# Performance work log

Measured on AMD Instinct MI355X. Metric: run time of the kernel, lower is better.

The kernel has to match this reference:

```python
import jax, jax.numpy as jnp
import numpy as np

N_POINTS = 2_000_000
GRID = (128, 128, 128)
N_COMP = 3


def _bspline_weights(u):
    # cubic B-spline basis, returns tuple of 4 arrays shaped like u
    u2 = u * u
    u3 = u2 * u
    w0 = (1.0 - u) ** 3 / 6.0
    w1 = (3.0 * u3 - 6.0 * u2 + 4.0) / 6.0
    w2 = (-3.0 * u3 + 3.0 * u2 + 3.0 * u + 1.0) / 6.0
    w3 = u3 / 6.0
    return (w0, w1, w2, w3)


def setup_inputs() -> dict:
    key = jax.random.key(0)
    kx, ky, kz, kp = jax.random.split(key, 4)
    # query points uniform in the supported domain [-1, 1]
    x = jax.random.uniform(kx, (N_POINTS,), jnp.float32, -1.0, 1.0)
    y = jax.random.uniform(ky, (N_POINTS,), jnp.float32, -1.0, 1.0)
    z = jax.random.uniform(kz, (N_POINTS,), jnp.float32, -1.0, 1.0)
    phi_x = jax.random.normal(kp, (*GRID, N_COMP), jnp.float32)
    return {"x": x, "y": y, "z": z, "phi_x": phi_x}


def reference(x, y, z, phi_x):
    # BSplineField3d.vectorized_displacement with support_outside=True,
    # default support_range=None -> spacing = 2/(n-3), origin = -1 - spacing.
    nx, ny, nz, _ = phi_x.shape
    dx = 2.0 / (nx - 3)
    dy = 2.0 / (ny - 3)
    dz = 2.0 / (nz - 3)
    ox, oy, oz = -1.0 - dx, -1.0 - dy, -1.0 - dz

    u = (x - ox - dx) / dx
    v = (y - oy - dy) / dy
    w = (z - oz - dz) / dz
    ix = jnp.floor(u).astype(jnp.int32)
    iy = jnp.floor(v).astype(jnp.int32)
    iz = jnp.floor(w).astype(jnp.int32)
    u = u - ix
    v = v - iy
    w = w - iz

    wu = _bspline_weights(u)
    wv = _bspline_weights(v)
    ww = _bspline_weights(w)

    T = jnp.zeros((x.shape[0], phi_x.shape[-1]), dtype=x.dtype)
    # 64 fixed taps: gather from control grid at clamped indices, MAC.
    for l in range(4):
        ixl = jnp.clip(ix + l, 0, nx - 1)
        for m in range(4):
            iym = jnp.clip(iy + m, 0, ny - 1)
            wum = wu[l] * wv[m]
            for n in range(4):
                izn = jnp.clip(iz + n, 0, nz - 1)
                coef = wum * ww[n]  # [N]
                T = T + coef[:, None] * phi_x[ixl, iym, izn]  # gather [N, C]
    return T
```

## Files before the change

kernel.cpp:

```cpp
#include <hip/hip_runtime.h>


#define NBINS 4096
#define NBLK  256

__device__ __forceinline__ void bspline_w(float u, float& w0, float& w1,
                                          float& w2, float& w3) {
    const float u2 = u * u;
    const float u3 = u2 * u;
    const float t  = 1.0f - u;
    w0 = t * t * t * (1.0f / 6.0f);
    w1 = (3.0f * u3 - 6.0f * u2 + 4.0f) * (1.0f / 6.0f);
    w2 = (-3.0f * u3 + 3.0f * u2 + 3.0f * u + 1.0f) * (1.0f / 6.0f);
    w3 = u3 * (1.0f / 6.0f);
}

__device__ __forceinline__ int point_bin(float x, float y, float z) {
    const float dx = 2.0f / 125.0f;
    const float ox = -1.0f - dx;
    const int ix = (int)floorf((x - ox - dx) / dx);
    const int iy = (int)floorf((y - ox - dx) / dx);
    const int iz = (int)floorf((z - ox - dx) / dx);
    const int bx = min(max(ix, 0), 127) >> 3;
    const int by = min(max(iy, 0), 127) >> 3;
    const int bz = min(max(iz, 0), 127) >> 3;
    return (bx << 8) | (by << 4) | bz;
}

__global__ __launch_bounds__(256) void hist_kernel(
    const float* __restrict__ xs, const float* __restrict__ ys,
    const float* __restrict__ zs, unsigned* __restrict__ hist,
    int n, int chunk) {
    __shared__ unsigned h[NBINS];
    for (int j = threadIdx.x; j < NBINS; j += 256) h[j] = 0;
    __syncthreads();
    const int b = blockIdx.x;
    const int lo = b * chunk;
    const int hi = min(n, lo + chunk);
    for (int i = lo + threadIdx.x; i < hi; i += 256)
        atomicAdd(&h[point_bin(xs[i], ys[i], zs[i])], 1u);
    __syncthreads();
    for (int j = threadIdx.x; j < NBINS; j += 256) hist[b * NBINS + j] = h[j];
}

__global__ __launch_bounds__(256) void colscan_kernel(
    unsigned* __restrict__ hist, unsigned* __restrict__ total) {
    const int j = blockIdx.x * 256 + threadIdx.x;
    unsigned run = 0;
#pragma unroll 8
    for (int b = 0; b < NBLK; ++b) {
        const unsigned c = hist[b * NBINS + j];
        hist[b * NBINS + j] = run;
        run += c;
    }
    total[j] = run;
}

__global__ __launch_bounds__(1024) void scan_kernel(
    const unsigned* __restrict__ total, unsigned* __restrict__ binbase) {
    __shared__ unsigned sdata[1024];
    const int t = threadIdx.x;
    const unsigned v0 = total[4 * t + 0];
    const unsigned v1 = total[4 * t + 1];
    const unsigned v2 = total[4 * t + 2];
    const unsigned v3 = total[4 * t + 3];
    sdata[t] = v0 + v1 + v2 + v3;
    __syncthreads();
    for (int off = 1; off < 1024; off <<= 1) {
        unsigned x = (t >= off) ? sdata[t - off] : 0u;
        __syncthreads();
        sdata[t] += x;
        __syncthreads();
    }
    const unsigned ex = (t > 0) ? sdata[t - 1] : 0u;
    binbase[4 * t + 0] = ex;
    binbase[4 * t + 1] = ex + v0;
    binbase[4 * t + 2] = ex + v0 + v1;
    binbase[4 * t + 3] = ex + v0 + v1 + v2;
}

__global__ __launch_bounds__(256) void scatter_kernel(
    const float* __restrict__ xs, const float* __restrict__ ys,
    const float* __restrict__ zs, const unsigned* __restrict__ hist,
    const unsigned* __restrict__ binbase, float4* __restrict__ rec,
    int n, int chunk) {
    __shared__ unsigned off[NBINS];
    const int b = blockIdx.x;
    for (int j = threadIdx.x; j < NBINS; j += 256)
        off[j] = hist[b * NBINS + j] + binbase[j];
    __syncthreads();
    const int lo = b * chunk;
    const int hi = min(n, lo + chunk);
    for (int i = lo + threadIdx.x; i < hi; i += 256) {
        const float x = xs[i], y = ys[i], z = zs[i];
        const unsigned p = atomicAdd(&off[point_bin(x, y, z)], 1u);
        rec[p] = make_float4(x, y, z, __int_as_float(i));
    }
}

__global__ __launch_bounds__(512) void eval_kernel(
    const float4* __restrict__ rec, const unsigned* __restrict__ binbase,
    const unsigned* __restrict__ total, const float* __restrict__ phi,
    float* __restrict__ out) {
    const int bin = blockIdx.x;
    const unsigned cnt = total[bin];
    if (cnt == 0) return;
    const unsigned start = binbase[bin];

    const int gx0 = ((bin >> 8) & 15) << 3;
    const int gy0 = ((bin >> 4) & 15) << 3;
    const int gz0 = (bin & 15) << 3;

    __shared__ float raw[121 * 36];
    __shared__ float4 W4[121 * 24];

    if (gz0 <= 112) {
        for (int p = threadIdx.x; p < 121 * 9; p += 512) {
            const int row = p / 9;
            const int q   = p - row * 9;
            const int lx = row / 11, ly = row - (row / 11) * 11;
            const int gx = min(gx0 + lx, 127);
            const int gy = min(gy0 + ly, 127);
            const float* src =
                phi + (size_t)((gx * 128 + gy) * 128 + gz0) * 3 + q * 4;
            *reinterpret_cast<float4*>(&raw[row * 36 + q * 4]) =
                *reinterpret_cast<const float4*>(src);
        }
    } else {
        for (int p = threadIdx.x; p < 121 * 11; p += 512) {
            const int row = p / 11;
            const int zz  = p - row * 11;
            const int lx = row / 11, ly = row - (row / 11) * 11;
            const int gx = min(gx0 + lx, 127);
            const int gy = min(gy0 + ly, 127);
            const int z  = min(gz0 + zz, 127);
            const float* s = phi + (size_t)((gx * 128 + gy) * 128 + z) * 3;
            raw[row * 36 + zz * 3 + 0] = s[0];
            raw[row * 36 + zz * 3 + 1] = s[1];
            raw[row * 36 + zz * 3 + 2] = s[2];
        }
    }
    __syncthreads();

    for (int p = threadIdx.x; p < 121 * 24; p += 512) {
        const int row = p / 24;
        const int t   = p - row * 24;
        const int s   = t / 3;
        const int c   = t - 3 * s;
        const float* r = &raw[row * 36 + s * 3 + c];
        W4[p] = make_float4(r[0], r[3], r[6], r[9]);
    }
    __syncthreads();

    const float dx = 2.0f / 125.0f;
    const float ox = -1.0f - dx;

    for (unsigned k = start + threadIdx.x; k < start + cnt; k += 512) {
        const float4 r4 = rec[k];
        const int idx = __float_as_int(r4.w);

        const float U = (r4.x - ox - dx) / dx;
        const float V = (r4.y - ox - dx) / dx;
        const float Z = (r4.z - ox - dx) / dx;
        const float fu = floorf(U), fv = floorf(V), fw = floorf(Z);
        const int ix = (int)fu, iy = (int)fv, iz = (int)fw;
        const float u = U - fu, v = V - fv, w = Z - fw;

        float wu[4], wv[4], wz[4];
        bspline_w(u, wu[0], wu[1], wu[2], wu[3]);
        bspline_w(v, wv[0], wv[1], wv[2], wv[3]);
        bspline_w(w, wz[0], wz[1], wz[2], wz[3]);

        int izb = iz < 0 ? 0 : iz;
        const bool sh = izb > 124;
        if (sh) izb = 124;
        const float zw0 = sh ? 0.0f : wz[0];
        const float zw1 = sh ? wz[0] : wz[1];
        const float zw2 = sh ? wz[1] : wz[2];
        const float zw3 = sh ? (wz[2] + wz[3]) : wz[3];
        const int lzb3 = (izb - gz0) * 3;

        int lxi[4], lyi[4];
#pragma unroll
        for (int l = 0; l < 4; ++l) {
            lxi[l] = min(max(ix + l, 0), 127) - gx0;
            lyi[l] = min(max(iy + l, 0), 127) - gy0;
        }

        float acc0 = 0.0f, acc1 = 0.0f, acc2 = 0.0f;
#pragma unroll
        for (int l = 0; l < 4; ++l) {
            const int rowx = lxi[l] * 11;
#pragma unroll
            for (int m = 0; m < 4; ++m) {
                const int base = (rowx + lyi[m]) * 24 + lzb3;
                const float4 a  = W4[base + 0];
                const float4 bb = W4[base + 1];
                const float4 cc = W4[base + 2];
                const float wm = wu[l] * wv[m];
                const float c0 = wm * zw0;
                const float c1 = wm * zw1;
                const float c2 = wm * zw2;
                const float c3 = wm * zw3;
                acc0 = fmaf(c0, a.x, acc0);
                acc0 = fmaf(c1, a.y, acc0);
                acc0 = fmaf(c2, a.z, acc0);
                acc0 = fmaf(c3, a.w, acc0);
                acc1 = fmaf(c0, bb.x, acc1);
                acc1 = fmaf(c1, bb.y, acc1);
                acc1 = fmaf(c2, bb.z, acc1);
                acc1 = fmaf(c3, bb.w, acc1);
                acc2 = fmaf(c0, cc.x, acc2);
                acc2 = fmaf(c1, cc.y, acc2);
                acc2 = fmaf(c2, cc.z, acc2);
                acc2 = fmaf(c3, cc.w, acc2);
            }
        }
        float* o = out + 3 * (size_t)idx;
        o[0] = acc0;
        o[1] = acc1;
        o[2] = acc2;
    }
}

__global__ __launch_bounds__(256) void bspline3d_direct(
    const float* __restrict__ xs, const float* __restrict__ ys,
    const float* __restrict__ zs, const float* __restrict__ phi,
    float* __restrict__ out, int n) {
    const int i = blockIdx.x * blockDim.x + threadIdx.x;
    if (i >= n) return;
    const float dx = 2.0f / 125.0f;
    const float ox = -1.0f - dx;
    float u = (xs[i] - ox - dx) / dx;
    float v = (ys[i] - ox - dx) / dx;
    float w = (zs[i] - ox - dx) / dx;
    const float fu = floorf(u), fv = floorf(v), fw = floorf(w);
    const int ix = (int)fu, iy = (int)fv, iz = (int)fw;
    u -= fu; v -= fv; w -= fw;
    float wu[4], wv[4], wz[4];
    bspline_w(u, wu[0], wu[1], wu[2], wu[3]);
    bspline_w(v, wv[0], wv[1], wv[2], wv[3]);
    bspline_w(w, wz[0], wz[1], wz[2], wz[3]);
    int izb = iz < 0 ? 0 : iz;
    const bool sh = izb > 124;
    if (sh) izb = 124;
    const float zw0 = sh ? 0.0f : wz[0];
    const float zw1 = sh ? wz[0] : wz[1];
    const float zw2 = sh ? wz[1] : wz[2];
    const float zw3 = sh ? (wz[2] + wz[3]) : wz[3];
    int xi[4], yi[4];
#pragma unroll
    for (int l = 0; l < 4; ++l) {
        xi[l] = min(max(ix + l, 0), 127);
        yi[l] = min(max(iy + l, 0), 127);
    }
    const float* pz = phi + izb * 3;
    float acc0 = 0.0f, acc1 = 0.0f, acc2 = 0.0f;
#pragma unroll
    for (int l = 0; l < 4; ++l) {
        const int rowx = xi[l] << 7;
#pragma unroll
        for (int m = 0; m < 4; ++m) {
            const float* p = pz + (rowx + yi[m]) * 384;
            const float4 a = *reinterpret_cast<const float4*>(p);
            const float4 b = *reinterpret_cast<const float4*>(p + 4);
            const float4 c = *reinterpret_cast<const float4*>(p + 8);
            const float wm = wu[l] * wv[m];
            const float c0 = wm * zw0, c1 = wm * zw1, c2 = wm * zw2, c3 = wm * zw3;
            acc0 = fmaf(c0, a.x, acc0); acc1 = fmaf(c0, a.y, acc1); acc2 = fmaf(c0, a.z, acc2);
            acc0 = fmaf(c1, a.w, acc0); acc1 = fmaf(c1, b.x, acc1); acc2 = fmaf(c1, b.y, acc2);
            acc0 = fmaf(c2, b.z, acc0); acc1 = fmaf(c2, b.w, acc1); acc2 = fmaf(c2, c.x, acc2);
            acc0 = fmaf(c3, c.y, acc0); acc1 = fmaf(c3, c.z, acc1); acc2 = fmaf(c3, c.w, acc2);
        }
    }
    float* o = out + 3 * (size_t)i;
    o[0] = acc0; o[1] = acc1; o[2] = acc2;
}

extern "C" void kernel_launch(void* const* d_in, const int* in_sizes, int n_in,
                              void* d_out, int out_size, void* d_ws,
                              size_t ws_size, hipStream_t stream) {
    const float* xs  = (const float*)d_in[0];
    const float* ys  = (const float*)d_in[1];
    const float* zs  = (const float*)d_in[2];
    const float* phi = (const float*)d_in[3];
    float* out = (float*)d_out;
    const int n = in_sizes[0];

    const size_t hist_off  = 0;
    const size_t total_off = hist_off + (size_t)NBLK * NBINS * 4;
    const size_t base_off  = total_off + NBINS * 4;
    const size_t rec_off   = base_off + NBINS * 4;
    const size_t need = rec_off + (size_t)n * 16;

    if (ws_size < need) {
        bspline3d_direct<<<(n + 255) / 256, 256, 0, stream>>>(xs, ys, zs, phi,
                                                              out, n);
        return;
    }

    unsigned* hist    = (unsigned*)((char*)d_ws + hist_off);
    unsigned* total   = (unsigned*)((char*)d_ws + total_off);
    unsigned* binbase = (unsigned*)((char*)d_ws + base_off);
    float4*   rec     = (float4*)((char*)d_ws + rec_off);

    const int chunk = (n + NBLK - 1) / NBLK;

    hist_kernel<<<NBLK, 256, 0, stream>>>(xs, ys, zs, hist, n, chunk);
    colscan_kernel<<<NBINS / 256, 256, 0, stream>>>(hist, total);
    scan_kernel<<<1, 1024, 0, stream>>>(total, binbase);
    scatter_kernel<<<NBLK, 256, 0, stream>>>(xs, ys, zs, hist, binbase, rec, n,
                                             chunk);
    eval_kernel<<<NBINS, 512, 0, stream>>>(rec, binbase, total, phi, out);
}
```

Baseline: 224.7 us.

## Widen binning kernels, vectorize point loads, shrink eval staging smem and pad stride

The histogram and scatter kernels move to 1024-thread blocks and read four points per thread with float4 loads. The chunk size is rounded to a multiple of four so those loads stay aligned. The eval kernel now stages the raw control-grid slab in 31-row pieces instead of all 121 rows, which cuts its shared memory. It also pads the transposed W4 row stride to 25 float4s to reduce bank conflicts, and adds a launch-bounds occupancy hint. The intent is more resident eval blocks and better memory throughput in the binning passes, at the cost of extra barrier rounds in eval staging.

```diff
diff --git a/kernel.cpp b/kernel.cpp
--- a/kernel.cpp
+++ b/kernel.cpp
@@ -3,6 +3,7 @@
 
 #define NBINS 4096
 #define NBLK  256
+#define W4STRIDE 25
 
 __device__ __forceinline__ void bspline_w(float u, float& w0, float& w1,
                                           float& w2, float& w3) {
@@ -27,27 +28,39 @@
     return (bx << 8) | (by << 4) | bz;
 }
 
-__global__ __launch_bounds__(256) void hist_kernel(
+__global__ __launch_bounds__(1024) void hist_kernel(
     const float* __restrict__ xs, const float* __restrict__ ys,
     const float* __restrict__ zs, unsigned* __restrict__ hist,
     int n, int chunk) {
     __shared__ unsigned h[NBINS];
-    for (int j = threadIdx.x; j < NBINS; j += 256) h[j] = 0;
+    for (int j = threadIdx.x; j < NBINS; j += 1024) h[j] = 0;
     __syncthreads();
     const int b = blockIdx.x;
     const int lo = b * chunk;
     const int hi = min(n, lo + chunk);
-    for (int i = lo + threadIdx.x; i < hi; i += 256)
-        atomicAdd(&h[point_bin(xs[i], ys[i], zs[i])], 1u);
+    for (int base = lo + threadIdx.x * 4; base < hi; base += 1024 * 4) {
+        if (base + 4 <= hi) {
+            const float4 x4 = *reinterpret_cast<const float4*>(xs + base);
+            const float4 y4 = *reinterpret_cast<const float4*>(ys + base);
+            const float4 z4 = *reinterpret_cast<const float4*>(zs + base);
+            atomicAdd(&h[point_bin(x4.x, y4.x, z4.x)], 1u);
+            atomicAdd(&h[point_bin(x4.y, y4.y, z4.y)], 1u);
+            atomicAdd(&h[point_bin(x4.z, y4.z, z4.z)], 1u);
+            atomicAdd(&h[point_bin(x4.w, y4.w, z4.w)], 1u);
+        } else {
+            for (int i = base; i < hi; ++i)
+                atomicAdd(&h[point_bin(xs[i], ys[i], zs[i])], 1u);
+        }
+    }
     __syncthreads();
-    for (int j = threadIdx.x; j < NBINS; j += 256) hist[b * NBINS + j] = h[j];
+    for (int j = threadIdx.x; j < NBINS; j += 1024) hist[b * NBINS + j] = h[j];
 }
 
 __global__ __launch_bounds__(256) void colscan_kernel(
     unsigned* __restrict__ hist, unsigned* __restrict__ total) {
     const int j = blockIdx.x * 256 + threadIdx.x;
     unsigned run = 0;
-#pragma unroll 8
+#pragma unroll 16
     for (int b = 0; b < NBLK; ++b) {
         const unsigned c = hist[b * NBINS + j];
         hist[b * NBINS + j] = run;
@@ -79,26 +92,43 @@
     binbase[4 * t + 3] = ex + v0 + v1 + v2;
 }
 
-__global__ __launch_bounds__(256) void scatter_kernel(
+__global__ __launch_bounds__(1024) void scatter_kernel(
     const float* __restrict__ xs, const float* __restrict__ ys,
     const float* __restrict__ zs, const unsigned* __restrict__ hist,
     const unsigned* __restrict__ binbase, float4* __restrict__ rec,
     int n, int chunk) {
     __shared__ unsigned off[NBINS];
     const int b = blockIdx.x;
-    for (int j = threadIdx.x; j < NBINS; j += 256)
+    for (int j = threadIdx.x; j < NBINS; j += 1024)
         off[j] = hist[b * NBINS + j] + binbase[j];
     __syncthreads();
     const int lo = b * chunk;
     const int hi = min(n, lo + chunk);
-    for (int i = lo + threadIdx.x; i < hi; i += 256) {
-        const float x = xs[i], y = ys[i], z = zs[i];
-        const unsigned p = atomicAdd(&off[point_bin(x, y, z)], 1u);
-        rec[p] = make_float4(x, y, z, __int_as_float(i));
-    }
-}
-
-__global__ __launch_bounds__(512) void eval_kernel(
+    for (int base = lo + threadIdx.x * 4; base < hi; base += 1024 * 4) {
+        if (base + 4 <= hi) {
+            const float4 x4 = *reinterpret_cast<const float4*>(xs + base);
+            const float4 y4 = *reinterpret_cast<const float4*>(ys + base);
+            const float4 z4 = *reinterpret_cast<const float4*>(zs + base);
+            unsigned p;
+            p = atomicAdd(&off[point_bin(x4.x, y4.x, z4.x)], 1u);
+            rec[p] = make_float4(x4.x, y4.x, z4.x, __int_as_float(base + 0));
+            p = atomicAdd(&off[point_bin(x4.y, y4.y, z4.y)], 1u);
+            rec[p] = make_float4(x4.y, y4.y, z4.y, __int_as_float(base + 1));
+            p = atomicAdd(&off[point_bin(x4.z, y4.z, z4.z)], 1u);
+            rec[p] = make_float4(x4.z, y4.z, z4.z, __int_as_float(base + 2));
+            p = atomicAdd(&off[point_bin(x4.w, y4.w, z4.w)], 1u);
+            rec[p] = make_float4(x4.w, y4.w, z4.w, __int_as_float(base + 3));
+        } else {
+            for (int i = base; i < hi; ++i) {
+                const float x = xs[i], y = ys[i], z = zs[i];
+                const unsigned p = atomicAdd(&off[point_bin(x, y, z)], 1u);
+                rec[p] = make_float4(x, y, z, __int_as_float(i));
+            }
+        }
+    }
+}
+
+__global__ __launch_bounds__(512, 6) void eval_kernel(
     const float4* __restrict__ rec, const unsigned* __restrict__ binbase,
     const unsigned* __restrict__ total, const float* __restrict__ phi,
     float* __restrict__ out) {
@@ -111,46 +141,46 @@
     const int gy0 = ((bin >> 4) & 15) << 3;
     const int gz0 = (bin & 15) << 3;
 
-    __shared__ float raw[121 * 36];
-    __shared__ float4 W4[121 * 24];
-
-    if (gz0 <= 112) {
-        for (int p = threadIdx.x; p < 121 * 9; p += 512) {
-            const int row = p / 9;
-            const int q   = p - row * 9;
-            const int lx = row / 11, ly = row - (row / 11) * 11;
-            const int gx = min(gx0 + lx, 127);
-            const int gy = min(gy0 + ly, 127);
-            const float* src =
-                phi + (size_t)((gx * 128 + gy) * 128 + gz0) * 3 + q * 4;
-            *reinterpret_cast<float4*>(&raw[row * 36 + q * 4]) =
-                *reinterpret_cast<const float4*>(src);
-        }
-    } else {
-        for (int p = threadIdx.x; p < 121 * 11; p += 512) {
-            const int row = p / 11;
-            const int zz  = p - row * 11;
-            const int lx = row / 11, ly = row - (row / 11) * 11;
-            const int gx = min(gx0 + lx, 127);
-            const int gy = min(gy0 + ly, 127);
-            const int z  = min(gz0 + zz, 127);
-            const float* s = phi + (size_t)((gx * 128 + gy) * 128 + z) * 3;
-            raw[row * 36 + zz * 3 + 0] = s[0];
-            raw[row * 36 + zz * 3 + 1] = s[1];
-            raw[row * 36 + zz * 3 + 2] = s[2];
-        }
-    }
-    __syncthreads();
-
-    for (int p = threadIdx.x; p < 121 * 24; p += 512) {
-        const int row = p / 24;
-        const int t   = p - row * 24;
-        const int s   = t / 3;
-        const int c   = t - 3 * s;
-        const float* r = &raw[row * 36 + s * 3 + c];
-        W4[p] = make_float4(r[0], r[3], r[6], r[9]);
-    }
-    __syncthreads();
+    __shared__ float raw[31 * 36];
+    __shared__ float4 W4[121 * W4STRIDE];
+
+    for (int r0 = 0; r0 < 121; r0 += 31) {
+        const int nr = min(31, 121 - r0);
+        if (gz0 <= 112) {
+            for (int p = threadIdx.x; p < nr * 9; p += 512) {
+                const int rr = p / 9, q = p - rr * 9;
+                const int row = r0 + rr;
+                const int lx = row / 11, ly = row - lx * 11;
+                const int gx = min(gx0 + lx, 127);
+                const int gy = min(gy0 + ly, 127);
+                const float* src =
+                    phi + (size_t)((gx * 128 + gy) * 128 + gz0) * 3 + q * 4;
+                *reinterpret_cast<float4*>(&raw[rr * 36 + q * 4]) =
+                    *reinterpret_cast<const float4*>(src);
+            }
+        } else {
+            for (int p = threadIdx.x; p < nr * 11; p += 512) {
+                const int rr = p / 11, zz = p - rr * 11;
+                const int row = r0 + rr;
+                const int lx = row / 11, ly = row - lx * 11;
+                const int gx = min(gx0 + lx, 127);
+                const int gy = min(gy0 + ly, 127);
+                const int z  = min(gz0 + zz, 127);
+                const float* s = phi + (size_t)((gx * 128 + gy) * 128 + z) * 3;
+                raw[rr * 36 + zz * 3 + 0] = s[0];
+                raw[rr * 36 + zz * 3 + 1] = s[1];
+                raw[rr * 36 + zz * 3 + 2] = s[2];
+            }
+        }
+        __syncthreads();
+        for (int p = threadIdx.x; p < nr * 24; p += 512) {
+            const int rr = p / 24, t = p - rr * 24;
+            const int s = t / 3, c = t - 3 * s;
+            const float* r = &raw[rr * 36 + s * 3 + c];
+            W4[(r0 + rr) * W4STRIDE + t] = make_float4(r[0], r[3], r[6], r[9]);
+        }
+        __syncthreads();
+    }
 
     const float dx = 2.0f / 125.0f;
     const float ox = -1.0f - dx;
@@ -193,7 +223,7 @@
             const int rowx = lxi[l] * 11;
 #pragma unroll
             for (int m = 0; m < 4; ++m) {
-                const int base = (rowx + lyi[m]) * 24 + lzb3;
+                const int base = (rowx + lyi[m]) * W4STRIDE + lzb3;
                 const float4 a  = W4[base + 0];
                 const float4 bb = W4[base + 1];
                 const float4 cc = W4[base + 2];
@@ -304,12 +334,12 @@
     unsigned* binbase = (unsigned*)((char*)d_ws + base_off);
     float4*   rec     = (float4*)((char*)d_ws + rec_off);
 
-    const int chunk = (n + NBLK - 1) / NBLK;
-
-    hist_kernel<<<NBLK, 256, 0, stream>>>(xs, ys, zs, hist, n, chunk);
+    const int chunk = (((n + NBLK - 1) / NBLK) + 3) & ~3;
+
+    hist_kernel<<<NBLK, 1024, 0, stream>>>(xs, ys, zs, hist, n, chunk);
     colscan_kernel<<<NBINS / 256, 256, 0, stream>>>(hist, total);
     scan_kernel<<<1, 1024, 0, stream>>>(total, binbase);
-    scatter_kernel<<<NBLK, 256, 0, stream>>>(xs, ys, zs, hist, binbase, rec, n,
-                                             chunk);
+    scatter_kernel<<<NBLK, 1024, 0, stream>>>(xs, ys, zs, hist, binbase, rec,
+                                              n, chunk);
     eval_kernel<<<NBINS, 512, 0, stream>>>(rec, binbase, total, phi, out);
 }
```

Measured after the change: 194.3 us. 1.16x faster.
